# Performance work log

Measured on AMD Instinct MI355X. Metric: run time of the kernel, lower is better.

The kernel has to match this reference:

```python
import jax, jax.numpy as jnp
import numpy as np

GAMMA = 2          # relu(cos_sim)**gamma, from init gamma=2
EPS = 1e-8         # torch CosineSimilarity eps (norm clamp)
B, C, H, WID = 4, 256, 64, 64


def setup_inputs() -> dict:
    key = jax.random.key(0)
    kx, kw = jax.random.split(key)
    x = jax.random.normal(kx, (B, C, H, WID), dtype=jnp.float32)
    # 1x1 conv (nlayers=1): weight [C_out, C_in], bias [C_out]
    W = jax.random.normal(kw, (C, C), dtype=jnp.float32) * 0.02
    b = jnp.zeros((C,), dtype=jnp.float32)
    return {"x": x, "W": W, "b": b}


def reference(x, W, b):
    # x: [B,C,H,W]. Flatten pixels: p/q index (h*W+w).
    Bs, Cs, Hs, Ws = x.shape
    xf = x.reshape(Bs, Cs, Hs * Ws)                      # [B,C,P]
    norm = jnp.sqrt(jnp.sum(xf * xf, axis=1, keepdims=True))
    xn = xf / jnp.maximum(norm, EPS)                     # channel-normalized
    # full pairwise cosine similarity over pixels, relu, power gamma
    s = jax.nn.relu(jnp.einsum('bcp,bcq->bpq', xn, xn)) ** GAMMA  # [B,P,Q]
    # transform: 1x1 conv = per-pixel linear map over channels
    gx = jnp.einsum('oc,bcp->bop', W, xf) + b[None, :, None]      # [B,C,P]
    # y[b,c,p] = sum_q s[b,p,q] * gx[b,c,q]  (== 'bijhw,bchw->bcij')
    y = jnp.einsum('bpq,bcq->bcp', s, gx)
    return y.reshape(Bs, Cs, Hs, Ws)
```

## Files before the change

kernel.cpp:

```cpp
#include <hip/hip_runtime.h>
#include <hip/hip_fp16.h>

#define BN 4
#define CN 256
#define PN 4096
#define QT 32
#define TSTR 264

typedef __attribute__((ext_vector_type(8))) short short8;
typedef __attribute__((ext_vector_type(8))) unsigned short ushort8;
typedef __attribute__((ext_vector_type(4))) unsigned short us4;
typedef __attribute__((ext_vector_type(4))) float f32x4;
typedef __attribute__((ext_vector_type(4))) unsigned int u32x4;
typedef unsigned int u32;

__device__ __forceinline__ unsigned short f2bf(float f) {
  u32 u = __builtin_bit_cast(u32, f);
  return (unsigned short)((u + 0x7fffu + ((u >> 16) & 1u)) >> 16);
}

__device__ __forceinline__ void async_copy16(const void* g, void* l) {
  __builtin_amdgcn_global_load_lds((const __attribute__((address_space(1))) u32*)g,
                                   (__attribute__((address_space(3))) u32*)l, 16, 0, 0);
}


__global__ __launch_bounds__(256) void k_nxgx(const float* __restrict__ x,
                                              const float* __restrict__ Wm,
                                              const float* __restrict__ bias,
                                              unsigned short* __restrict__ xnK,
                                              unsigned short* __restrict__ gxF) {
  __shared__ unsigned short tl[64 * TSTR];
  __shared__ float red[4][64];
  __shared__ float mnl[64];
  const int b = blockIdx.y, qb = blockIdx.x;
  const int tid = threadIdx.x;
  const int tp = tid & 63, cg = tid >> 6;

  {
    const float* xp = x + ((size_t)b * CN + cg * 64) * PN + qb * 64 + tp;
    float v[64];
    float ss = 0.f;
#pragma unroll
    for (int i = 0; i < 64; ++i) {
      v[i] = xp[(size_t)i * PN];
      ss += v[i] * v[i];
    }
    red[cg][tp] = ss;
    __syncthreads();
    float nrm = sqrtf(red[0][tp] + red[1][tp] + red[2][tp] + red[3][tp]);
    float mn = fmaxf(nrm, 1e-8f);
    float rn = 1.f / mn;
    if (cg == 0) mnl[tp] = mn;
    unsigned int* tl32 = (unsigned int*)tl;
#pragma unroll
    for (int j = 0; j < 32; ++j) {
      unsigned int w = (unsigned int)f2bf(v[2 * j] * rn) |
                       ((unsigned int)f2bf(v[2 * j + 1] * rn) << 16);
      tl32[tp * (TSTR / 2) + cg * 32 + j] = w;
    }
    __syncthreads();
    char* dstb = (char*)xnK + (size_t)b * (PN * CN * 2) + (size_t)qb * 32768;
#pragma unroll
    for (int m = 0; m < 8; ++m) {
      int idx = m * 256 + tid;
      int F = idx >> 6, ln = idx & 63;
      int pl = (F >> 3) * 16 + (ln & 15);
      int ch = (F & 7) * 32 + (ln >> 4) * 8;
      ushort8 o = *(const ushort8*)(tl + pl * TSTR + ch);
      *(ushort8*)(dstb + (size_t)idx * 16) = o;
    }
  }

  const int wave = tid >> 6, lane = tid & 63;
  const int lr = lane & 15, g = lane >> 4;
  char* vbb = (char*)gxF + (size_t)b * (PN * CN * 2) + (size_t)qb * 32768;
#pragma unroll
  for (int mp = 0; mp < 2; ++mp) {
    short8 af[2][8];
#pragma unroll
    for (int mt = 0; mt < 2; ++mt) {
      const float* wr = Wm + (size_t)(wave * 64 + mp * 32 + mt * 16 + lr) * CN;
#pragma unroll
      for (int k = 0; k < 8; ++k) {
        const float* ap = wr + k * 32 + g * 8;
        short8 a;
#pragma unroll
        for (int j = 0; j < 8; ++j) a[j] = (short)f2bf(ap[j]);
        af[mt][k] = a;
      }
    }
    f32x4 acc[2][4];
#pragma unroll
    for (int mt = 0; mt < 2; ++mt)
#pragma unroll
      for (int n = 0; n < 4; ++n) acc[mt][n] = (f32x4){0.f, 0.f, 0.f, 0.f};
#pragma unroll
    for (int n = 0; n < 4; ++n)
#pragma unroll
      for (int k = 0; k < 8; ++k) {
        short8 bf = *(const short8*)((const char*)tl + (n * 16 + lr) * (TSTR * 2) + k * 64 + g * 16);
        acc[0][n] = __builtin_amdgcn_mfma_f32_16x16x32_bf16(af[0][k], bf, acc[0][n], 0, 0, 0);
        acc[1][n] = __builtin_amdgcn_mfma_f32_16x16x32_bf16(af[1][k], bf, acc[1][n], 0, 0, 0);
      }
#pragma unroll
    for (int n = 0; n < 4; ++n) {
      float mn = mnl[n * 16 + lr];
      int kk = n >> 1;
      int q32 = (n & 1) * 16 + lr;
      int gp = (q32 >> 2) & 3;
      int j = ((q32 >> 4) & 1) * 4 + (q32 & 3);
#pragma unroll
      for (int mt = 0; mt < 2; ++mt)
#pragma unroll
        for (int i = 0; i < 4; ++i) {
          int c = wave * 64 + mp * 32 + mt * 16 + g * 4 + i;
          float v = acc[mt][n][i] * mn + bias[c];
          *(unsigned short*)(vbb + ((kk * 16 + (c >> 4)) << 10) + (gp << 8) + ((c & 15) << 4) + (j << 1)) = f2bf(v);
        }
    }
  }
}

extern __shared__ char smem[];

__global__ __launch_bounds__(512, 4) void k_attn(const unsigned short* __restrict__ xnK,
                                                 const unsigned short* __restrict__ gxF,
                                                 __half* __restrict__ p0h, __half* __restrict__ p1h,
                                                 __half* __restrict__ p2h, __half* __restrict__ p3h,
                                                 int lq, int ntiles) {
  const int fid = blockIdx.x;
  const int b = fid & 3;
  const int qs = (fid >> 2) & ((1 << lq) - 1);
  const int pblk = fid >> (2 + lq);
  const int tid = threadIdx.x;
  const int wave = tid >> 6, lane = tid & 63, lr = lane & 15, g = lane >> 4;
  const int qt0 = (qs * (PN >> lq)) >> 5;
  const int p0 = pblk * 128 + wave * 16;
  __half* dsth = (qs == 0) ? p0h : (qs == 1) ? p1h : (qs == 2) ? p2h : p3h;

  const char* xb = (const char*)xnK + (size_t)b * (PN * CN * 2);
  const char* vg = (const char*)gxF + (size_t)b * (PN * CN * 2);
  const char* kq = xb + (size_t)qt0 * 16384;
  const char* vq = vg + (size_t)qt0 * 16384;
  const int ldst = tid * 16;
  const int lane16 = lane * 16;

  auto issue = [&](int t) {
    char* kb = smem + (t & 1) * 32768;
    const char* ks = kq + (size_t)t * 16384 + ldst;
    const char* vs = vq + (size_t)t * 16384 + ldst;
    async_copy16(ks, kb + ldst);
    async_copy16(ks + 8192, kb + ldst + 8192);
    async_copy16(vs, kb + 16384 + ldst);
    async_copy16(vs + 8192, kb + 16384 + ldst + 8192);
  };

  issue(0);

  short8 qf[8];
  {
    const char* qpb = xb + (size_t)(pblk * 2 + (wave >> 2)) * 32768;
    const int ntp = wave & 3;
#pragma unroll
    for (int k = 0; k < 8; ++k)
      qf[k] = *(const short8*)(qpb + ((ntp * 8 + k) << 10) + ((g * 16 + lr) << 4));
  }

  f32x4 yacc[16];
#pragma unroll
  for (int n = 0; n < 16; ++n) yacc[n] = (f32x4){0.f, 0.f, 0.f, 0.f};

  for (int t = 0; t < ntiles; ++t) {
    const char* kb = smem + (t & 1) * 32768;
    const char* vb = kb + 16384;

    asm volatile("s_waitcnt vmcnt(0)" ::: "memory");
    __builtin_amdgcn_s_barrier();
    if (t + 1 < ntiles) issue(t + 1);

    f32x4 sacc0 = (f32x4){0.f, 0.f, 0.f, 0.f};
    f32x4 sacc1 = (f32x4){0.f, 0.f, 0.f, 0.f};
    __builtin_amdgcn_s_setprio(1);
#pragma unroll
    for (int k = 0; k < 8; ++k) {
      short8 kf0 = *(const short8*)(kb + k * 1024 + lane16);
      short8 kf1 = *(const short8*)(kb + (8 + k) * 1024 + lane16);
      sacc0 = __builtin_amdgcn_mfma_f32_16x16x32_bf16(kf0, qf[k], sacc0, 0, 0, 0);
      sacc1 = __builtin_amdgcn_mfma_f32_16x16x32_bf16(kf1, qf[k], sacc1, 0, 0, 0);
    }
    __builtin_amdgcn_s_setprio(0);

    u32 pa[4];
#pragma unroll
    for (int h = 0; h < 2; ++h) {
      float a0 = fmaxf(sacc0[2 * h], 0.f); a0 *= a0;
      float a1 = fmaxf(sacc0[2 * h + 1], 0.f); a1 *= a1;
      asm("v_cvt_pk_bf16_f32 %0, %1, %2" : "=v"(pa[h]) : "v"(a0), "v"(a1));
      float b0 = fmaxf(sacc1[2 * h], 0.f); b0 *= b0;
      float b1 = fmaxf(sacc1[2 * h + 1], 0.f); b1 *= b1;
      asm("v_cvt_pk_bf16_f32 %0, %1, %2" : "=v"(pa[2 + h]) : "v"(b0), "v"(b1));
    }
    u32x4 w0 = {pa[0], pa[1], pa[2], pa[3]};
    short8 a0 = __builtin_bit_cast(short8, w0);

    __builtin_amdgcn_s_setprio(1);
#pragma unroll
    for (int n2 = 0; n2 < 16; ++n2) {
      short8 vf = *(const short8*)(vb + n2 * 1024 + lane16);
      yacc[n2] = __builtin_amdgcn_mfma_f32_16x16x32_bf16(a0, vf, yacc[n2], 0, 0, 0);
    }
    __builtin_amdgcn_s_setprio(0);
  }
  asm volatile("s_waitcnt vmcnt(0)" ::: "memory");
  __builtin_amdgcn_s_barrier();

  float* yl = (float*)(smem + wave * 8192);
  const int cq = lane >> 2, pq = (lane & 3) << 2;
#pragma unroll
  for (int cc = 0; cc < 4; ++cc) {
#pragma unroll
    for (int nn = 0; nn < 4; ++nn)
#pragma unroll
      for (int i = 0; i < 4; ++i)
        yl[(nn * 16 + lr) * 17 + g * 4 + i] = yacc[cc * 4 + nn][i];
#pragma unroll
    for (int i2 = 0; i2 < 4; ++i2) {
      int c = i2 * 16 + cq;
      float4 v = *(const float4*)(yl + c * 17 + pq);
      size_t off = ((size_t)b * CN + cc * 64 + c) * PN + p0 + pq;
      us4 h;
      h[0] = __builtin_bit_cast(unsigned short, __float2half(v.x));
      h[1] = __builtin_bit_cast(unsigned short, __float2half(v.y));
      h[2] = __builtin_bit_cast(unsigned short, __float2half(v.z));
      h[3] = __builtin_bit_cast(unsigned short, __float2half(v.w));
      *(us4*)(dsth + off) = h;
    }
  }
}

__global__ void k_add(float* __restrict__ o, const uint2* __restrict__ a,
                      const uint2* __restrict__ bb, const uint2* __restrict__ c,
                      const uint2* __restrict__ d, int np, int n4) {
  int i = blockIdx.x * blockDim.x + threadIdx.x;
  int stride = gridDim.x * blockDim.x;
  float4* o4 = (float4*)o;
  for (; i < n4; i += stride) {
    uint2 ua = a[i];
    float2 f0 = __half22float2(__builtin_bit_cast(__half2, ua.x));
    float2 f1 = __half22float2(__builtin_bit_cast(__half2, ua.y));
    float4 r = {f0.x, f0.y, f1.x, f1.y};
    uint2 ub = bb[i];
    f0 = __half22float2(__builtin_bit_cast(__half2, ub.x));
    f1 = __half22float2(__builtin_bit_cast(__half2, ub.y));
    r.x += f0.x; r.y += f0.y; r.z += f1.x; r.w += f1.y;
    if (np > 2) {
      uint2 uc = c[i];
      f0 = __half22float2(__builtin_bit_cast(__half2, uc.x));
      f1 = __half22float2(__builtin_bit_cast(__half2, uc.y));
      r.x += f0.x; r.y += f0.y; r.z += f1.x; r.w += f1.y;
      uint2 ud = d[i];
      f0 = __half22float2(__builtin_bit_cast(__half2, ud.x));
      f1 = __half22float2(__builtin_bit_cast(__half2, ud.y));
      r.x += f0.x; r.y += f0.y; r.z += f1.x; r.w += f1.y;
    }
    o4[i] = r;
  }
}

extern "C" void kernel_launch(void* const* d_in, const int* in_sizes, int n_in,
                              void* d_out, int out_size, void* d_ws, size_t ws_size,
                              hipStream_t stream) {
  const float* x = (const float*)d_in[0];
  const float* Wm = (const float*)d_in[1];
  const float* bias = (const float*)d_in[2];
  float* out = (float*)d_out;

  char* ws = (char*)d_ws;
  unsigned short* xnK = (unsigned short*)ws;
  unsigned short* gxF = (unsigned short*)(ws + (size_t)8388608);
  __half* p0 = (__half*)(ws + (size_t)16777216);
  __half* p1 = p0 + 4194304;
  __half* p2 = p1 + 4194304;
  __half* p3 = p2 + 4194304;
  const size_t need4 = 16777216ULL + 4ULL * 8388608ULL;

  hipFuncSetAttribute(reinterpret_cast<const void*>(k_attn),
                      hipFuncAttributeMaxDynamicSharedMemorySize, 65536);

  k_nxgx<<<dim3(PN / 64, BN), 256, 0, stream>>>(x, Wm, bias, xnK, gxF);
  if (ws_size >= need4) {
    k_attn<<<dim3(512), 512, 65536, stream>>>(xnK, gxF, p0, p1, p2, p3, 2, (PN / 4) / QT);
    k_add<<<dim3(1024), 256, 0, stream>>>(out, (const uint2*)p0, (const uint2*)p1,
                                          (const uint2*)p2, (const uint2*)p3, 4, BN * CN * PN / 4);
  } else {
    k_attn<<<dim3(256), 512, 65536, stream>>>(xnK, gxF, p0, p1, p0, p1, 1, (PN / 2) / QT);
    k_add<<<dim3(1024), 256, 0, stream>>>(out, (const uint2*)p0, (const uint2*)p1,
                                          (const uint2*)p0, (const uint2*)p1, 2, BN * CN * PN / 4);
  }
}
```

Measured before the change: 100.3 us.

## Switch attention kernel to 32x32 MFMA tiles with triple-buffered K/V prefetch

Reworks the attention kernel so each wave handles 32 query pixels using 32x32x16 bf16 MFMA for both the similarity and value products. The K and V layouts written by the producer kernel change to match the new fragment shapes. Three LDS buffers now allow loads to run two tiles ahead. The block count is halved so each block covers twice as many pixels. This aims to reduce LDS fragment reads per FLOP and to hide load latency, but it halves the grid to 256 blocks, which may leave some CUs on the MI355X under-occupied, and it raises register and LDS pressure.

```diff
diff --git a/kernel.cpp b/kernel.cpp
--- a/kernel.cpp
+++ b/kernel.cpp
@@ -11,6 +11,7 @@
 typedef __attribute__((ext_vector_type(8))) unsigned short ushort8;
 typedef __attribute__((ext_vector_type(4))) unsigned short us4;
 typedef __attribute__((ext_vector_type(4))) float f32x4;
+typedef __attribute__((ext_vector_type(16))) float f32x16;
 typedef __attribute__((ext_vector_type(4))) unsigned int u32x4;
 typedef unsigned int u32;
 
@@ -64,10 +65,8 @@
 #pragma unroll
     for (int m = 0; m < 8; ++m) {
       int idx = m * 256 + tid;
-      int F = idx >> 6, ln = idx & 63;
-      int pl = (F >> 3) * 16 + (ln & 15);
-      int ch = (F & 7) * 32 + (ln >> 4) * 8;
-      ushort8 o = *(const ushort8*)(tl + pl * TSTR + ch);
+      int blk = idx >> 10, kc = (idx >> 6) & 15, l = idx & 63;
+      ushort8 o = *(const ushort8*)(tl + (blk * 32 + (l & 31)) * TSTR + kc * 16 + (l >> 5) * 8);
       *(ushort8*)(dstb + (size_t)idx * 16) = o;
     }
   }
@@ -75,6 +74,8 @@
   const int wave = tid >> 6, lane = tid & 63;
   const int lr = lane & 15, g = lane >> 4;
   char* vbb = (char*)gxF + (size_t)b * (PN * CN * 2) + (size_t)qb * 32768;
+  const int lh = (lr >> 2) & 1;
+  const int jj = (lr & 3) | (((lr >> 3) & 1) << 2);
 #pragma unroll
   for (int mp = 0; mp < 2; ++mp) {
     short8 af[2][8];
@@ -106,17 +107,16 @@
 #pragma unroll
     for (int n = 0; n < 4; ++n) {
       float mn = mnl[n * 16 + lr];
-      int kk = n >> 1;
-      int q32 = (n & 1) * 16 + lr;
-      int gp = (q32 >> 2) & 3;
-      int j = ((q32 >> 4) & 1) * 4 + (q32 & 3);
+      int blk = n >> 1, chunk = n & 1;
 #pragma unroll
       for (int mt = 0; mt < 2; ++mt)
 #pragma unroll
         for (int i = 0; i < 4; ++i) {
           int c = wave * 64 + mp * 32 + mt * 16 + g * 4 + i;
           float v = acc[mt][n][i] * mn + bias[c];
-          *(unsigned short*)(vbb + ((kk * 16 + (c >> 4)) << 10) + (gp << 8) + ((c & 15) << 4) + (j << 1)) = f2bf(v);
+          int byteoff = blk * 16384 + ((((c >> 5) & 7) * 2 + chunk) << 10) +
+                        (((lh << 5) | (c & 31)) << 4) + (jj << 1);
+          *(unsigned short*)(vbb + byteoff) = f2bf(v);
         }
     }
   }
@@ -124,7 +124,7 @@
 
 extern __shared__ char smem[];
 
-__global__ __launch_bounds__(512, 4) void k_attn(const unsigned short* __restrict__ xnK,
+__global__ __launch_bounds__(512, 2) void k_attn(const unsigned short* __restrict__ xnK,
                                                  const unsigned short* __restrict__ gxF,
                                                  __half* __restrict__ p0h, __half* __restrict__ p1h,
                                                  __half* __restrict__ p2h, __half* __restrict__ p3h,
@@ -134,107 +134,111 @@
   const int qs = (fid >> 2) & ((1 << lq) - 1);
   const int pblk = fid >> (2 + lq);
   const int tid = threadIdx.x;
-  const int wave = tid >> 6, lane = tid & 63, lr = lane & 15, g = lane >> 4;
+  const int wave = tid >> 6, lane = tid & 63;
+  const int l31 = lane & 31, h = lane >> 5;
   const int qt0 = (qs * (PN >> lq)) >> 5;
-  const int p0 = pblk * 128 + wave * 16;
+  const int p0w = pblk * 256 + wave * 32;
   __half* dsth = (qs == 0) ? p0h : (qs == 1) ? p1h : (qs == 2) ? p2h : p3h;
 
   const char* xb = (const char*)xnK + (size_t)b * (PN * CN * 2);
-  const char* vg = (const char*)gxF + (size_t)b * (PN * CN * 2);
+  const char* vgb = (const char*)gxF + (size_t)b * (PN * CN * 2);
   const char* kq = xb + (size_t)qt0 * 16384;
-  const char* vq = vg + (size_t)qt0 * 16384;
+  const char* vq = vgb + (size_t)qt0 * 16384;
   const int ldst = tid * 16;
   const int lane16 = lane * 16;
 
   auto issue = [&](int t) {
-    char* kb = smem + (t & 1) * 32768;
+    char* buf = smem + (t % 3) * 32768;
     const char* ks = kq + (size_t)t * 16384 + ldst;
     const char* vs = vq + (size_t)t * 16384 + ldst;
-    async_copy16(ks, kb + ldst);
-    async_copy16(ks + 8192, kb + ldst + 8192);
-    async_copy16(vs, kb + 16384 + ldst);
-    async_copy16(vs + 8192, kb + 16384 + ldst + 8192);
+    async_copy16(ks, buf + ldst);
+    async_copy16(ks + 8192, buf + ldst + 8192);
+    async_copy16(vs, buf + 16384 + ldst);
+    async_copy16(vs + 8192, buf + 16384 + ldst + 8192);
   };
 
+  short8 qf[16];
+  {
+    const char* qpb = xb + (size_t)(pblk * 8 + wave) * 16384;
+#pragma unroll
+    for (int kc = 0; kc < 16; ++kc)
+      qf[kc] = *(const short8*)(qpb + (kc << 10) + lane16);
+  }
+  asm volatile("s_waitcnt vmcnt(0)" ::: "memory");
   issue(0);
-
-  short8 qf[8];
-  {
-    const char* qpb = xb + (size_t)(pblk * 2 + (wave >> 2)) * 32768;
-    const int ntp = wave & 3;
-#pragma unroll
-    for (int k = 0; k < 8; ++k)
-      qf[k] = *(const short8*)(qpb + ((ntp * 8 + k) << 10) + ((g * 16 + lr) << 4));
-  }
-
-  f32x4 yacc[16];
-#pragma unroll
-  for (int n = 0; n < 16; ++n) yacc[n] = (f32x4){0.f, 0.f, 0.f, 0.f};
+  issue(1);
+
+  f32x16 yacc[8];
+#pragma unroll
+  for (int ct = 0; ct < 8; ++ct)
+#pragma unroll
+    for (int r = 0; r < 16; ++r) yacc[ct][r] = 0.f;
 
   for (int t = 0; t < ntiles; ++t) {
-    const char* kb = smem + (t & 1) * 32768;
+    const char* kb = smem + (t % 3) * 32768;
     const char* vb = kb + 16384;
 
-    asm volatile("s_waitcnt vmcnt(0)" ::: "memory");
+    if (t + 1 < ntiles) {
+      asm volatile("s_waitcnt vmcnt(4)" ::: "memory");
+    } else {
+      asm volatile("s_waitcnt vmcnt(0)" ::: "memory");
+    }
     __builtin_amdgcn_s_barrier();
-    if (t + 1 < ntiles) issue(t + 1);
-
-    f32x4 sacc0 = (f32x4){0.f, 0.f, 0.f, 0.f};
-    f32x4 sacc1 = (f32x4){0.f, 0.f, 0.f, 0.f};
+    if (t + 2 < ntiles) issue(t + 2);
+
+    f32x16 sacc;
+#pragma unroll
+    for (int r = 0; r < 16; ++r) sacc[r] = 0.f;
     __builtin_amdgcn_s_setprio(1);
 #pragma unroll
-    for (int k = 0; k < 8; ++k) {
-      short8 kf0 = *(const short8*)(kb + k * 1024 + lane16);
-      short8 kf1 = *(const short8*)(kb + (8 + k) * 1024 + lane16);
-      sacc0 = __builtin_amdgcn_mfma_f32_16x16x32_bf16(kf0, qf[k], sacc0, 0, 0, 0);
-      sacc1 = __builtin_amdgcn_mfma_f32_16x16x32_bf16(kf1, qf[k], sacc1, 0, 0, 0);
+    for (int kc = 0; kc < 16; ++kc) {
+      short8 kf = *(const short8*)(kb + (kc << 10) + lane16);
+      sacc = __builtin_amdgcn_mfma_f32_32x32x16_bf16(kf, qf[kc], sacc, 0, 0, 0);
     }
     __builtin_amdgcn_s_setprio(0);
 
-    u32 pa[4];
-#pragma unroll
-    for (int h = 0; h < 2; ++h) {
-      float a0 = fmaxf(sacc0[2 * h], 0.f); a0 *= a0;
-      float a1 = fmaxf(sacc0[2 * h + 1], 0.f); a1 *= a1;
-      asm("v_cvt_pk_bf16_f32 %0, %1, %2" : "=v"(pa[h]) : "v"(a0), "v"(a1));
-      float b0 = fmaxf(sacc1[2 * h], 0.f); b0 *= b0;
-      float b1 = fmaxf(sacc1[2 * h + 1], 0.f); b1 *= b1;
-      asm("v_cvt_pk_bf16_f32 %0, %1, %2" : "=v"(pa[2 + h]) : "v"(b0), "v"(b1));
-    }
-    u32x4 w0 = {pa[0], pa[1], pa[2], pa[3]};
-    short8 a0 = __builtin_bit_cast(short8, w0);
+    u32 pw[8];
+#pragma unroll
+    for (int w = 0; w < 8; ++w) {
+      float x0 = fmaxf(sacc[2 * w], 0.f); x0 *= x0;
+      float x1 = fmaxf(sacc[2 * w + 1], 0.f); x1 *= x1;
+      asm("v_cvt_pk_bf16_f32 %0, %1, %2" : "=v"(pw[w]) : "v"(x0), "v"(x1));
+    }
+    u32x4 wa = {pw[0], pw[1], pw[2], pw[3]};
+    u32x4 wb = {pw[4], pw[5], pw[6], pw[7]};
+    short8 aa = __builtin_bit_cast(short8, wa);
+    short8 ab = __builtin_bit_cast(short8, wb);
 
     __builtin_amdgcn_s_setprio(1);
 #pragma unroll
-    for (int n2 = 0; n2 < 16; ++n2) {
-      short8 vf = *(const short8*)(vb + n2 * 1024 + lane16);
-      yacc[n2] = __builtin_amdgcn_mfma_f32_16x16x32_bf16(a0, vf, yacc[n2], 0, 0, 0);
+    for (int ct = 0; ct < 8; ++ct) {
+      short8 vfa = *(const short8*)(vb + ((ct * 2) << 10) + lane16);
+      yacc[ct] = __builtin_amdgcn_mfma_f32_32x32x16_bf16(aa, vfa, yacc[ct], 0, 0, 0);
+      short8 vfb = *(const short8*)(vb + ((ct * 2 + 1) << 10) + lane16);
+      yacc[ct] = __builtin_amdgcn_mfma_f32_32x32x16_bf16(ab, vfb, yacc[ct], 0, 0, 0);
     }
     __builtin_amdgcn_s_setprio(0);
   }
-  asm volatile("s_waitcnt vmcnt(0)" ::: "memory");
   __builtin_amdgcn_s_barrier();
 
-  float* yl = (float*)(smem + wave * 8192);
-  const int cq = lane >> 2, pq = (lane & 3) << 2;
-#pragma unroll
-  for (int cc = 0; cc < 4; ++cc) {
-#pragma unroll
-    for (int nn = 0; nn < 4; ++nn)
-#pragma unroll
-      for (int i = 0; i < 4; ++i)
-        yl[(nn * 16 + lr) * 17 + g * 4 + i] = yacc[cc * 4 + nn][i];
+  float* yl = (float*)(smem + wave * 4352);
+#pragma unroll
+  for (int ct = 0; ct < 8; ++ct) {
+#pragma unroll
+    for (int r = 0; r < 16; ++r)
+      yl[l31 * 33 + ((r & 3) + 8 * (r >> 2) + 4 * h)] = yacc[ct][r];
 #pragma unroll
     for (int i2 = 0; i2 < 4; ++i2) {
-      int c = i2 * 16 + cq;
-      float4 v = *(const float4*)(yl + c * 17 + pq);
-      size_t off = ((size_t)b * CN + cc * 64 + c) * PN + p0 + pq;
-      us4 h;
-      h[0] = __builtin_bit_cast(unsigned short, __float2half(v.x));
-      h[1] = __builtin_bit_cast(unsigned short, __float2half(v.y));
-      h[2] = __builtin_bit_cast(unsigned short, __float2half(v.z));
-      h[3] = __builtin_bit_cast(unsigned short, __float2half(v.w));
-      *(us4*)(dsth + off) = h;
+      int c_l = i2 * 8 + (lane >> 3);
+      int p4 = (lane & 7) * 4;
+      float4 v = *(const float4*)(yl + c_l * 33 + p4);
+      size_t off = ((size_t)b * CN + ct * 32 + c_l) * PN + p0w + p4;
+      us4 h4;
+      h4[0] = __builtin_bit_cast(unsigned short, __float2half(v.x));
+      h4[1] = __builtin_bit_cast(unsigned short, __float2half(v.y));
+      h4[2] = __builtin_bit_cast(unsigned short, __float2half(v.z));
+      h4[3] = __builtin_bit_cast(unsigned short, __float2half(v.w));
+      *(us4*)(dsth + off) = h4;
     }
   }
 }
@@ -286,15 +290,15 @@
   const size_t need4 = 16777216ULL + 4ULL * 8388608ULL;
 
   hipFuncSetAttribute(reinterpret_cast<const void*>(k_attn),
-                      hipFuncAttributeMaxDynamicSharedMemorySize, 65536);
+                      hipFuncAttributeMaxDynamicSharedMemorySize, 98304);
 
   k_nxgx<<<dim3(PN / 64, BN), 256, 0, stream>>>(x, Wm, bias, xnK, gxF);
   if (ws_size >= need4) {
-    k_attn<<<dim3(512), 512, 65536, stream>>>(xnK, gxF, p0, p1, p2, p3, 2, (PN / 4) / QT);
+    k_attn<<<dim3(256), 512, 98304, stream>>>(xnK, gxF, p0, p1, p2, p3, 2, (PN / 4) / QT);
     k_add<<<dim3(1024), 256, 0, stream>>>(out, (const uint2*)p0, (const uint2*)p1,
                                           (const uint2*)p2, (const uint2*)p3, 4, BN * CN * PN / 4);
   } else {
-    k_attn<<<dim3(256), 512, 65536, stream>>>(xnK, gxF, p0, p1, p0, p1, 1, (PN / 2) / QT);
+    k_attn<<<dim3(128), 512, 98304, stream>>>(xnK, gxF, p0, p1, p0, p1, 1, (PN / 2) / QT);
     k_add<<<dim3(1024), 256, 0, stream>>>(out, (const uint2*)p0, (const uint2*)p1,
                                           (const uint2*)p0, (const uint2*)p1, 2, BN * CN * PN / 4);
   }
```

Result: no change. 101.3 us (+1.0%).
